# Performance work log

Measured on AMD Instinct MI355X. Metric: run time of the kernel, lower is better.

Reference implementation:

```python
import jax, jax.numpy as jnp
import numpy as np

N_NODES = 131072
N_EDGES = 2097152
B = 256
NODES_PER_GRAPH = 512  # uniform graphs -> to_dense_batch == reshape
F_IN = 74
D = 128
L = 3
EPS = 1e-5


def setup_inputs() -> dict:
    key = jax.random.key(0)
    ks = jax.random.split(key, 12)
    x = jax.random.normal(ks[0], (N_NODES, F_IN), dtype=jnp.float32)
    edge_index = jax.random.randint(ks[1], (2, N_EDGES), 0, N_NODES, dtype=jnp.int32)
    batch = (jnp.arange(N_NODES, dtype=jnp.int32) // NODES_PER_GRAPH)
    s = 1.0 / np.sqrt(D)
    W_init = jax.random.uniform(ks[2], (F_IN, D), jnp.float32, -s, s)
    W_gcn = jax.random.uniform(ks[3], (L, D, D), jnp.float32, -s, s)
    b_gcn = jnp.zeros((L, D), jnp.float32)
    gamma = jnp.ones((L, D), jnp.float32)
    beta = jnp.zeros((L, D), jnp.float32)
    W_res = jax.random.uniform(ks[4], (L, D, D), jnp.float32, -s, s)
    b_res = jax.random.uniform(ks[5], (L, D), jnp.float32, -s, s)
    return {"x": x, "edge_index": edge_index, "batch": batch, "W_init": W_init,
            "W_gcn": W_gcn, "b_gcn": b_gcn, "gamma": gamma, "beta": beta,
            "W_res": W_res, "b_res": b_res}


def _gcn_conv(x, src, tgt, norm, W, b):
    # PyG GCNConv: h = x @ W ; out[tgt] += norm * h[src] ; + bias
    h = x @ W                                    # [N, D]
    msg = h[src] * norm[:, None]                 # [E+N, D] gather (memory-bound)
    out = jax.ops.segment_sum(msg, tgt, num_segments=N_NODES)
    return out + b


def _batchnorm(x, g, bta):
    mean = jnp.mean(x, axis=0)
    var = jnp.var(x, axis=0)  # biased, matches torch BN training forward
    return (x - mean) * jax.lax.rsqrt(var + EPS) * g + bta


def reference(x, edge_index, batch, W_init, W_gcn, b_gcn, gamma, beta, W_res, b_res):
    # add self loops once; symmetric deg^{-1/2} normalization (PyG default)
    loops = jnp.arange(N_NODES, dtype=edge_index.dtype)
    src = jnp.concatenate([edge_index[0], loops])
    tgt = jnp.concatenate([edge_index[1], loops])
    deg = jax.ops.segment_sum(jnp.ones_like(src, dtype=jnp.float32), tgt,
                              num_segments=N_NODES)
    dinv = jnp.where(deg > 0, jax.lax.rsqrt(jnp.maximum(deg, 1.0)), 0.0)
    norm = dinv[src] * dinv[tgt]

    h = x @ W_init                               # init_transform (no bias)
    for i in range(L):
        conv = _gcn_conv(h, src, tgt, norm, W_gcn[i], b_gcn[i])
        h_new = jax.nn.relu(_batchnorm(conv, gamma[i], beta[i]))
        h = h_new + (h @ W_res[i] + b_res[i])
    # to_dense_batch with uniform NODES_PER_GRAPH -> reshape, all mask=True
    return h.reshape(B, NODES_PER_GRAPH, D)
```

## Files before the change

kernel.cpp:

```cpp
#include <hip/hip_runtime.h>

#define NN 131072
#define NE 2097152
#define DD 128
#define LL 3

#define NB 256
#define BSH 9
#define TILE (NE / NB)

typedef __attribute__((ext_vector_type(8))) short short8;
typedef __attribute__((ext_vector_type(4))) float f32x4;

__device__ __forceinline__ ushort f2bf(float f) {
    uint u = __float_as_uint(f);
    return (ushort)((u + 0x7fffu + ((u >> 16) & 1u)) >> 16);
}
__device__ __forceinline__ float bflo(uint u) { return __uint_as_float(u << 16); }
__device__ __forceinline__ float bfhi(uint u) { return __uint_as_float(u & 0xffff0000u); }

__global__ __launch_bounds__(256) void k_prep(const float* __restrict__ x,
                                              const float* __restrict__ Wi,
                                              const float* __restrict__ Wg,
                                              const float* __restrict__ Wr,
                                              uint* __restrict__ xb,
                                              ushort* __restrict__ wt,
                                              float* __restrict__ bns) {
    const int t = threadIdx.x, blk = blockIdx.x;
    const size_t id = (size_t)blk * 256 + t;
    const int n = (int)(id >> 6);
    const int k0 = (int)(id & 63) * 2;
    float v0 = (k0 < 74) ? x[(size_t)n * 74 + k0] : 0.0f;
    float v1 = (k0 + 1 < 74) ? x[(size_t)n * 74 + k0 + 1] : 0.0f;
    xb[id] = (uint)f2bf(v0) | ((uint)f2bf(v1) << 16);
    if (blk < 448) {
        const int id2 = blk * 256 + t;
        const int m = id2 >> 14;
        const int c = (id2 >> 7) & 127;
        const int k = id2 & 127;
        float v;
        if (m == 0)      v = (k < 74) ? Wi[k * DD + c] : 0.0f;
        else if (m <= 3) v = Wg[(size_t)(m - 1) * DD * DD + k * DD + c];
        else             v = Wr[(size_t)(m - 4) * DD * DD + k * DD + c];
        wt[id2] = f2bf(v);
    }
    if (blk == 448) {
        bns[t] = 0.0f; bns[t + 256] = 0.0f; bns[t + 512] = 0.0f;
    }
}

__global__ __launch_bounds__(256) void kA_count(const int* __restrict__ tgt,
                                                int* __restrict__ blockHist) {
    __shared__ int hist[NB];
    const int t = threadIdx.x, blk = blockIdx.x;
    hist[t] = 0;
    __syncthreads();
    const int base = blk * TILE;
#pragma unroll 8
    for (int j = 0; j < TILE / 256; ++j)
        atomicAdd(&hist[tgt[base + j * 256 + t] >> BSH], 1);
    __syncthreads();
    blockHist[t * NB + blk] = hist[t];
}

__global__ __launch_bounds__(256) void kA_scan1(int* __restrict__ blockHist,
                                                int* __restrict__ rowSum) {
    __shared__ int sc[256];
    const int t = threadIdx.x, b = blockIdx.x;
    const int v = blockHist[b * NB + t];
    sc[t] = v;
    __syncthreads();
    for (int off = 1; off < 256; off <<= 1) {
        int a = sc[t];
        int u = (t >= off) ? sc[t - off] : 0;
        __syncthreads();
        sc[t] = a + u;
        __syncthreads();
    }
    blockHist[b * NB + t] = sc[t] - v;
    if (t == 255) rowSum[b] = sc[255];
}

__global__ __launch_bounds__(256) void kA_scatter(const int* __restrict__ src,
                                                  const int* __restrict__ tgt,
                                                  const int* __restrict__ chunkBase,
                                                  const int* __restrict__ rowSum,
                                                  int* __restrict__ bstart,
                                                  uint* __restrict__ packed) {
    __shared__ int cur[NB];
    __shared__ int sc[256];
    const int t = threadIdx.x, blk = blockIdx.x;
    const int v = rowSum[t];
    sc[t] = v;
    __syncthreads();
    for (int off = 1; off < 256; off <<= 1) {
        int a = sc[t];
        int u = (t >= off) ? sc[t - off] : 0;
        __syncthreads();
        sc[t] = a + u;
        __syncthreads();
    }
    const int bst = sc[t] - v;
    cur[t] = bst + chunkBase[t * NB + blk];
    if (blk == 0) {
        bstart[t] = bst;
        if (t == 255) bstart[NB] = sc[255];
    }
    __syncthreads();
    const int base = blk * TILE;
#pragma unroll 4
    for (int j = 0; j < TILE / 256; ++j) {
        const int e = base + j * 256 + t;
        const int tg = tgt[e], s = src[e];
        const int b = tg >> BSH;
        const int pos = atomicAdd(&cur[b], 1);
        packed[pos] = (uint)s | ((uint)(tg & ((1 << BSH) - 1)) << 17);
    }
}

__global__ __launch_bounds__(256) void kB_sort(const uint* __restrict__ packed,
                                               const int* __restrict__ bstart,
                                               int* __restrict__ rowp,
                                               float* __restrict__ dinv,
                                               int* __restrict__ deg,
                                               int* __restrict__ ssrc) {
    __shared__ int cnt[1 << BSH];
    __shared__ int pscan[256];
    const int t = threadIdx.x, b = blockIdx.x;
    const int e0 = bstart[b], e1 = bstart[b + 1];
    cnt[t] = 0; cnt[t + 256] = 0;
    __syncthreads();
    for (int e = e0 + t; e < e1; e += 256)
        atomicAdd(&cnt[packed[e] >> 17], 1);
    __syncthreads();
    const int c0 = cnt[2 * t], c1 = cnt[2 * t + 1];
    pscan[t] = c0 + c1;
    __syncthreads();
    for (int off = 1; off < 256; off <<= 1) {
        int v = pscan[t];
        int u = (t >= off) ? pscan[t - off] : 0;
        __syncthreads();
        pscan[t] = v + u;
        __syncthreads();
    }
    const int ex0 = pscan[t] - c0 - c1;
    const int ex1 = ex0 + c0;
    const int n0 = (b << BSH) + 2 * t;
    rowp[n0] = e0 + ex0;
    rowp[n0 + 1] = e0 + ex1;
    dinv[n0] = rsqrtf((float)(c0 + 1));
    dinv[n0 + 1] = rsqrtf((float)(c1 + 1));
    deg[n0] = c0 + 1;
    deg[n0 + 1] = c1 + 1;
    if (b == NB - 1 && t == 255) rowp[NN] = e1;
    __syncthreads();
    cnt[2 * t] = ex0;
    cnt[2 * t + 1] = ex1;
    __syncthreads();
    for (int e = e0 + t; e < e1; e += 256) {
        const uint p = packed[e];
        const int tl = p >> 17;
        const int pos = atomicAdd(&cnt[tl], 1);
        ssrc[e0 + pos] = (int)(p & 0x1FFFFu);
    }
}

__global__ __launch_bounds__(256) void k_pack(int* __restrict__ ssrc,
                                              const int* __restrict__ deg) {
    const int e = blockIdx.x * 256 + threadIdx.x;
    const int s = ssrc[e];
    ssrc[e] = s | (deg[s] << 17);
}

#define STAGE_A(buf, rowbase)                                                  \
    for (int ch = w * 4; ch < w * 4 + 4; ++ch) {                               \
        const int row_ = ch * 4 + lr;                                          \
        const int kb_ = (lc * 16) ^ ((row_ & 7) << 4);                         \
        const ushort* srcA_ = A + ((rowbase) + row_) * DD + (kb_ >> 1);        \
        __builtin_amdgcn_global_load_lds(                                      \
            (const __attribute__((address_space(1))) void*)srcA_,              \
            (__attribute__((address_space(3))) void*)(As[buf] + ch * 512),     \
            16, 0, 0);                                                         \
    }

template <int MODE>
__global__ __launch_bounds__(256) void k_mgemm(const ushort* __restrict__ A,
                                               const ushort* __restrict__ Bt,
                                               ushort* outb,
                                               float* __restrict__ outf,
                                               const ushort* __restrict__ convb,
                                               const float* __restrict__ gamma,
                                               const float* __restrict__ beta,
                                               const float* __restrict__ bres,
                                               float* __restrict__ bnsums) {
    __shared__ ushort Bs[16384];
    __shared__ ushort As[2][8192];
    __shared__ float sred[256];
    const int t = threadIdx.x;
    const int w = t >> 6, l = t & 63;
    const int lc = l & 15, lr = l >> 4;
    const size_t base0 = (size_t)blockIdx.x * 256;

    for (int ch = w * 8; ch < w * 8 + 8; ++ch) {
        const int row = ch * 4 + lr;
        const int kb = (lc * 16) ^ ((row & 7) << 4);
        const ushort* srcB = Bt + (size_t)row * DD + (kb >> 1);
        __builtin_amdgcn_global_load_lds(
            (const __attribute__((address_space(1))) void*)srcB,
            (__attribute__((address_space(3))) void*)(Bs + ch * 512), 16, 0, 0);
    }
    STAGE_A(0, base0);
    if (MODE >= 2 && t < DD) {
        const float invN = 1.0f / (float)NN;
        const float mean = bnsums[t] * invN;
        const float var = bnsums[DD + t] * invN - mean * mean;
        const float sc = gamma[t] * rsqrtf(var + 1e-5f);
        sred[t] = sc;
        sred[DD + t] = beta[t] - mean * sc;
    }
    __syncthreads();

    float scv[8], shv[8], bbv[8];
    if (MODE >= 2) {
#pragma unroll
        for (int n = 0; n < 8; ++n) {
            const int c = n * 16 + lc;
            scv[n] = sred[c]; shv[n] = sred[DD + c]; bbv[n] = bres[c];
        }
    }
    float ps[8] = {}, ps2[8] = {};

    int cur = 0;
    for (int tt = 0; tt < 4; ++tt) {
        const size_t row0 = base0 + tt * 64;
        if (tt < 3) STAGE_A(cur ^ 1, row0 + 64);

        f32x4 acc[8] = {};
        const char* Ab = (const char*)As[cur];
        const char* Bb = (const char*)Bs;
#pragma unroll
        for (int kk = 0; kk < 4; ++kk) {
            const int kb = kk * 64 + lr * 16;
            const int r = w * 16 + lc;
            const short8 a = *(const short8*)(Ab + r * 256 + (kb ^ ((r & 7) << 4)));
#pragma unroll
            for (int n = 0; n < 8; ++n) {
                const int c = n * 16 + lc;
                short8 b = *(const short8*)(Bb + c * 256 + (kb ^ ((c & 7) << 4)));
                acc[n] = __builtin_amdgcn_mfma_f32_16x16x32_bf16(a, b, acc[n], 0, 0, 0);
            }
        }

        if (MODE == 0) {
#pragma unroll
            for (int n = 0; n < 8; ++n) {
                const int c = n * 16 + lc;
#pragma unroll
                for (int j = 0; j < 4; ++j) {
                    const size_t r = row0 + w * 16 + lr * 4 + j;
                    outb[r * DD + c] = f2bf(acc[n][j]);
                }
            }
        } else if (MODE == 1) {
#pragma unroll
            for (int n = 0; n < 8; ++n) {
                const int c = n * 16 + lc;
#pragma unroll
                for (int j = 0; j < 4; ++j) {
                    const size_t r = row0 + w * 16 + lr * 4 + j;
                    const float v = acc[n][j];
                    outb[r * DD + c] = f2bf(v);
                    ps[n] += v; ps2[n] += v * v;
                }
            }
        } else {
#pragma unroll
            for (int n = 0; n < 8; ++n) {
                const int c = n * 16 + lc;
#pragma unroll
                for (int j = 0; j < 4; ++j) {
                    const size_t r = row0 + w * 16 + lr * 4 + j;
                    const float cv = __uint_as_float((uint)convb[r * DD + c] << 16);
                    const float v = fmaxf(cv * scv[n] + shv[n], 0.0f) + acc[n][j] + bbv[n];
                    if (MODE == 2) outb[r * DD + c] = f2bf(v);
                    if (MODE == 3) outf[r * DD + c] = v;
                }
            }
        }
        __syncthreads();
        cur ^= 1;
    }

    if (MODE == 1) {
        sred[t] = 0.0f;
        __syncthreads();
#pragma unroll
        for (int n = 0; n < 8; ++n) {
            const int c = n * 16 + lc;
            atomicAdd(&sred[c], ps[n]);
            atomicAdd(&sred[DD + c], ps2[n]);
        }
        __syncthreads();
        atomicAdd(&bnsums[t], sred[t]);
    }
}

__global__ __launch_bounds__(256) void k_aggregate(const int* __restrict__ rowp,
                                                   const float* __restrict__ dinv,
                                                   const int* __restrict__ ssrc,
                                                   const uint* __restrict__ hb,
                                                   uint* __restrict__ aggb) {
    __shared__ float2 eb[4][64];
    const int wv = threadIdx.x >> 6;
    const int n = blockIdx.x * 4 + wv;
    const int l = threadIdx.x & 63;
    const float dn = dinv[n];
    const uint u0 = hb[((uint)n << 6) + l];
    const float dn2 = dn * dn;
    float ax = dn2 * bflo(u0), ay = dn2 * bfhi(u0);
    const int e0 = rowp[n], e1 = rowp[n + 1];
    for (int base = e0; base < e1; base += 64) {
        const int cnt = min(64, e1 - base);
        float nm = 0.0f; uint sb = 0;
        if (l < cnt) {
            const uint p = (uint)__builtin_nontemporal_load(ssrc + base + l);
            sb = (p & 0x1FFFFu) << 6;
            nm = dn * rsqrtf((float)(p >> 17));
        }
        eb[wv][l] = make_float2(nm, __uint_as_float(sb));
        int i = 0;
        for (; i + 16 <= cnt; i += 16) {
            uint vv[16]; float nmv[16];
#pragma unroll
            for (int j = 0; j < 16; ++j) {
                const float2 e = eb[wv][i + j];
                nmv[j] = e.x;
                vv[j] = hb[__float_as_uint(e.y) + l];
            }
#pragma unroll
            for (int j = 0; j < 16; ++j) {
                ax += nmv[j] * bflo(vv[j]);
                ay += nmv[j] * bfhi(vv[j]);
            }
        }
        for (; i < cnt; i += 8) {
            uint vv[8]; float nmv[8];
#pragma unroll
            for (int j = 0; j < 8; ++j) {
                const float2 e = eb[wv][i + j];
                nmv[j] = e.x;
                vv[j] = hb[__float_as_uint(e.y) + l];
            }
#pragma unroll
            for (int j = 0; j < 8; ++j) {
                ax += nmv[j] * bflo(vv[j]);
                ay += nmv[j] * bfhi(vv[j]);
            }
        }
    }
    aggb[((uint)n << 6) + l] = (uint)f2bf(ax) | ((uint)f2bf(ay) << 16);
}

extern "C" void kernel_launch(void* const* d_in, const int* in_sizes, int n_in,
                              void* d_out, int out_size, void* d_ws, size_t ws_size,
                              hipStream_t stream) {
    const float* x      = (const float*)d_in[0];
    const int*   ei     = (const int*)d_in[1];
    const float* W_init = (const float*)d_in[3];
    const float* W_gcn  = (const float*)d_in[4];
    const float* gamma  = (const float*)d_in[6];
    const float* beta   = (const float*)d_in[7];
    const float* W_res  = (const float*)d_in[8];
    const float* b_res  = (const float*)d_in[9];

    float* h = (float*)d_out;
    char* p = (char*)d_ws;
    ushort* aggb = (ushort*)p;           p += (size_t)NN * DD * 2;
    ushort* hb   = (ushort*)p;           p += (size_t)NN * DD * 2;
    ushort* convb = (ushort*)p;          p += (size_t)NN * DD * 2;
    uint*   xb   = (uint*)convb;
    float*  dinv = (float*)p;            p += (size_t)NN * 4;
    int*    deg  = (int*)p;              p += (size_t)NN * 4;
    float*  bns  = (float*)p;            p += 768 * 4;
    ushort* wt   = (ushort*)p;           p += 7 * 16384 * 2;
    int* blockHist = (int*)p;            p += (size_t)NB * NB * 4;
    int* rowSum  = (int*)p;              p += NB * 4;
    int* bstart  = (int*)p;              p += (NB + 1) * 4 + 4;
    uint* packed = (uint*)p;             p += (size_t)NE * 4;
    int* rowp    = (int*)p;              p += ((size_t)NN + 1) * 4 + 4;
    int* ssrc    = (int*)p;

    const int* srcp = ei;
    const int* tgtp = ei + NE;

    k_prep<<<NN * 64 / 256, 256, 0, stream>>>(x, W_init, W_gcn, W_res, xb, wt, bns);
    kA_count<<<NB, 256, 0, stream>>>(tgtp, blockHist);
    kA_scan1<<<NB, 256, 0, stream>>>(blockHist, rowSum);
    kA_scatter<<<NB, 256, 0, stream>>>(srcp, tgtp, blockHist, rowSum, bstart, packed);
    kB_sort<<<NB, 256, 0, stream>>>(packed, bstart, rowp, dinv, deg, ssrc);
    k_pack<<<NE / 256, 256, 0, stream>>>(ssrc, deg);

    k_mgemm<0><<<NN / 256, 256, 0, stream>>>((const ushort*)xb, wt, hb,
                                             nullptr, nullptr, nullptr, nullptr,
                                             nullptr, nullptr);

    for (int i = 0; i < LL; ++i) {
        k_aggregate<<<NN / 4, 256, 0, stream>>>(rowp, dinv, ssrc,
                                                (const uint*)hb, (uint*)aggb);
        k_mgemm<1><<<NN / 256, 256, 0, stream>>>(aggb, wt + (size_t)(1 + i) * 16384,
                                                 convb, nullptr, nullptr, nullptr,
                                                 nullptr, nullptr, bns + i * 256);
        if (i < LL - 1)
            k_mgemm<2><<<NN / 256, 256, 0, stream>>>(hb, wt + (size_t)(4 + i) * 16384,
                                                     hb, nullptr, convb,
                                                     gamma + i * DD, beta + i * DD,
                                                     b_res + i * DD, bns + i * 256);
        else
            k_mgemm<3><<<NN / 256, 256, 0, stream>>>(hb, wt + (size_t)(4 + i) * 16384,
                                                     nullptr, h, convb,
                                                     gamma + i * DD, beta + i * DD,
                                                     b_res + i * DD, bns + i * 256);
    }
}
```

Measured before the change: 471.7 us.

## Fuse sparse aggregation with GCN weight GEMM and BN stats into one kernel

Result: slower. 546.3 us (+15.8%).

```diff
diff --git a/kernel.cpp b/kernel.cpp
--- a/kernel.cpp
+++ b/kernel.cpp
@@ -228,7 +228,6 @@
             scv[n] = sred[c]; shv[n] = sred[DD + c]; bbv[n] = bres[c];
         }
     }
-    float ps[8] = {}, ps2[8] = {};
 
     int cur = 0;
     for (int tt = 0; tt < 4; ++tt) {
@@ -259,18 +258,6 @@
                 for (int j = 0; j < 4; ++j) {
                     const size_t r = row0 + w * 16 + lr * 4 + j;
                     outb[r * DD + c] = f2bf(acc[n][j]);
-                }
-            }
-        } else if (MODE == 1) {
-#pragma unroll
-            for (int n = 0; n < 8; ++n) {
-                const int c = n * 16 + lc;
-#pragma unroll
-                for (int j = 0; j < 4; ++j) {
-                    const size_t r = row0 + w * 16 + lr * 4 + j;
-                    const float v = acc[n][j];
-                    outb[r * DD + c] = f2bf(v);
-                    ps[n] += v; ps2[n] += v * v;
                 }
             }
         } else {
@@ -290,75 +277,120 @@
         __syncthreads();
         cur ^= 1;
     }
-
-    if (MODE == 1) {
-        sred[t] = 0.0f;
-        __syncthreads();
-#pragma unroll
-        for (int n = 0; n < 8; ++n) {
-            const int c = n * 16 + lc;
-            atomicAdd(&sred[c], ps[n]);
-            atomicAdd(&sred[DD + c], ps2[n]);
-        }
-        __syncthreads();
-        atomicAdd(&bnsums[t], sred[t]);
-    }
-}
-
-__global__ __launch_bounds__(256) void k_aggregate(const int* __restrict__ rowp,
-                                                   const float* __restrict__ dinv,
-                                                   const int* __restrict__ ssrc,
-                                                   const uint* __restrict__ hb,
-                                                   uint* __restrict__ aggb) {
-    __shared__ float2 eb[4][64];
-    const int wv = threadIdx.x >> 6;
-    const int n = blockIdx.x * 4 + wv;
-    const int l = threadIdx.x & 63;
-    const float dn = dinv[n];
-    const uint u0 = hb[((uint)n << 6) + l];
-    const float dn2 = dn * dn;
-    float ax = dn2 * bflo(u0), ay = dn2 * bfhi(u0);
-    const int e0 = rowp[n], e1 = rowp[n + 1];
-    for (int base = e0; base < e1; base += 64) {
-        const int cnt = min(64, e1 - base);
-        float nm = 0.0f; uint sb = 0;
-        if (l < cnt) {
-            const uint p = (uint)__builtin_nontemporal_load(ssrc + base + l);
-            sb = (p & 0x1FFFFu) << 6;
-            nm = dn * rsqrtf((float)(p >> 17));
-        }
-        eb[wv][l] = make_float2(nm, __uint_as_float(sb));
-        int i = 0;
-        for (; i + 16 <= cnt; i += 16) {
-            uint vv[16]; float nmv[16];
-#pragma unroll
-            for (int j = 0; j < 16; ++j) {
-                const float2 e = eb[wv][i + j];
-                nmv[j] = e.x;
-                vv[j] = hb[__float_as_uint(e.y) + l];
-            }
-#pragma unroll
-            for (int j = 0; j < 16; ++j) {
-                ax += nmv[j] * bflo(vv[j]);
-                ay += nmv[j] * bfhi(vv[j]);
-            }
-        }
-        for (; i < cnt; i += 8) {
-            uint vv[8]; float nmv[8];
-#pragma unroll
-            for (int j = 0; j < 8; ++j) {
-                const float2 e = eb[wv][i + j];
-                nmv[j] = e.x;
-                vv[j] = hb[__float_as_uint(e.y) + l];
-            }
-#pragma unroll
-            for (int j = 0; j < 8; ++j) {
-                ax += nmv[j] * bflo(vv[j]);
-                ay += nmv[j] * bfhi(vv[j]);
-            }
-        }
-    }
-    aggb[((uint)n << 6) + l] = (uint)f2bf(ax) | ((uint)f2bf(ay) << 16);
+}
+
+__global__ __launch_bounds__(512) void k_aggemm(const int* __restrict__ rowp,
+                                                const float* __restrict__ dinv,
+                                                const int* __restrict__ ssrc,
+                                                const uint* __restrict__ hb,
+                                                const ushort* __restrict__ Bt,
+                                                ushort* __restrict__ convb,
+                                                float* __restrict__ bnsums) {
+    __shared__ ushort Ag[8192];
+    __shared__ ushort Bs[16384];
+    __shared__ float2 eb[8][64];
+    __shared__ float sred[256];
+    const int t = threadIdx.x;
+    const int w = t >> 6, l = t & 63;
+    const int lc = l & 15, lr = l >> 4;
+    const int base0 = blockIdx.x * 64;
+
+    for (int ch = w * 4; ch < w * 4 + 4; ++ch) {
+        const int row = ch * 4 + lr;
+        const int kb = (lc * 16) ^ ((row & 7) << 4);
+        const ushort* srcB = Bt + (size_t)row * DD + (kb >> 1);
+        __builtin_amdgcn_global_load_lds(
+            (const __attribute__((address_space(1))) void*)srcB,
+            (__attribute__((address_space(3))) void*)(Bs + ch * 512), 16, 0, 0);
+    }
+    if (t < 256) sred[t] = 0.0f;
+
+    for (int ni = 0; ni < 8; ++ni) {
+        const int nl = w * 8 + ni;
+        const int n = base0 + nl;
+        const float dn = dinv[n];
+        const uint u0 = hb[((uint)n << 6) + l];
+        const float dn2 = dn * dn;
+        float ax = dn2 * bflo(u0), ay = dn2 * bfhi(u0);
+        const int e0 = rowp[n], e1 = rowp[n + 1];
+        for (int base = e0; base < e1; base += 64) {
+            const int cnt = min(64, e1 - base);
+            float nm = 0.0f; uint sb = 0;
+            if (l < cnt) {
+                const uint p = (uint)__builtin_nontemporal_load(ssrc + base + l);
+                sb = (p & 0x1FFFFu) << 6;
+                nm = dn * rsqrtf((float)(p >> 17));
+            }
+            eb[w][l] = make_float2(nm, __uint_as_float(sb));
+            int i = 0;
+            for (; i + 16 <= cnt; i += 16) {
+                uint vv[16]; float nmv[16];
+#pragma unroll
+                for (int j = 0; j < 16; ++j) {
+                    const float2 e = eb[w][i + j];
+                    nmv[j] = e.x;
+                    vv[j] = hb[__float_as_uint(e.y) + l];
+                }
+#pragma unroll
+                for (int j = 0; j < 16; ++j) {
+                    ax += nmv[j] * bflo(vv[j]);
+                    ay += nmv[j] * bfhi(vv[j]);
+                }
+            }
+            for (; i < cnt; i += 8) {
+                uint vv[8]; float nmv[8];
+#pragma unroll
+                for (int j = 0; j < 8; ++j) {
+                    const float2 e = eb[w][i + j];
+                    nmv[j] = e.x;
+                    vv[j] = hb[__float_as_uint(e.y) + l];
+                }
+#pragma unroll
+                for (int j = 0; j < 8; ++j) {
+                    ax += nmv[j] * bflo(vv[j]);
+                    ay += nmv[j] * bfhi(vv[j]);
+                }
+            }
+        }
+        const uint ov = (uint)f2bf(ax) | ((uint)f2bf(ay) << 16);
+        *(uint*)((char*)Ag + nl * 256 + ((4 * l) ^ ((nl & 7) << 4))) = ov;
+    }
+    __syncthreads();
+
+    f32x4 acc[4] = {};
+    const char* Ab = (const char*)Ag;
+    const char* Bb = (const char*)Bs;
+    const int rg = (w & 3) * 16;
+    const int cg = (w >> 2) * 64;
+#pragma unroll
+    for (int kk = 0; kk < 4; ++kk) {
+        const int kb = kk * 64 + lr * 16;
+        const int r = rg + lc;
+        const short8 a = *(const short8*)(Ab + r * 256 + (kb ^ ((r & 7) << 4)));
+#pragma unroll
+        for (int n2 = 0; n2 < 4; ++n2) {
+            const int c = cg + n2 * 16 + lc;
+            short8 b = *(const short8*)(Bb + c * 256 + (kb ^ ((c & 7) << 4)));
+            acc[n2] = __builtin_amdgcn_mfma_f32_16x16x32_bf16(a, b, acc[n2], 0, 0, 0);
+        }
+    }
+
+#pragma unroll
+    for (int n2 = 0; n2 < 4; ++n2) {
+        const int c = cg + n2 * 16 + lc;
+        float ps = 0.0f, ps2 = 0.0f;
+#pragma unroll
+        for (int j = 0; j < 4; ++j) {
+            const size_t r = (size_t)base0 + rg + lr * 4 + j;
+            const float v = acc[n2][j];
+            convb[r * DD + c] = f2bf(v);
+            ps += v; ps2 += v * v;
+        }
+        atomicAdd(&sred[c], ps);
+        atomicAdd(&sred[DD + c], ps2);
+    }
+    __syncthreads();
+    if (t < 256) atomicAdd(&bnsums[t], sred[t]);
 }
 
 extern "C" void kernel_launch(void* const* d_in, const int* in_sizes, int n_in,
@@ -375,7 +407,6 @@
 
     float* h = (float*)d_out;
     char* p = (char*)d_ws;
-    ushort* aggb = (ushort*)p;           p += (size_t)NN * DD * 2;
     ushort* hb   = (ushort*)p;           p += (size_t)NN * DD * 2;
     ushort* convb = (ushort*)p;          p += (size_t)NN * DD * 2;
     uint*   xb   = (uint*)convb;
@@ -405,11 +436,9 @@
                                              nullptr, nullptr);
 
     for (int i = 0; i < LL; ++i) {
-        k_aggregate<<<NN / 4, 256, 0, stream>>>(rowp, dinv, ssrc,
-                                                (const uint*)hb, (uint*)aggb);
-        k_mgemm<1><<<NN / 256, 256, 0, stream>>>(aggb, wt + (size_t)(1 + i) * 16384,
-                                                 convb, nullptr, nullptr, nullptr,
-                                                 nullptr, nullptr, bns + i * 256);
+        k_aggemm<<<NN / 64, 512, 0, stream>>>(rowp, dinv, ssrc, (const uint*)hb,
+                                              wt + (size_t)(1 + i) * 16384,
+                                              convb, bns + i * 256);
         if (i < LL - 1)
             k_mgemm<2><<<NN / 256, 256, 0, stream>>>(hb, wt + (size_t)(4 + i) * 16384,
                                                      hb, nullptr, convb,
```
